# Optimization experiments

Hardware: AMD Instinct MI355X
Metric: run time of the kernel (lower is better)

Reference implementation:

```python
import jax, jax.numpy as jnp
import numpy as np

EMB = 64
HID = 64


def setup_inputs() -> dict:
    key = jax.random.key(0)
    ks = jax.random.split(key, 7)
    obs_len, batch = 20, 65536
    s_in = 1.0 / np.sqrt(2.0)   # torch Linear init scale
    s_h = 1.0 / np.sqrt(HID)    # torch LSTM init scale
    return {
        "obs_traj": jax.random.normal(ks[0], (obs_len, batch, 2), dtype=jnp.float32),
        "W_emb": jax.random.uniform(ks[1], (EMB, 2), jnp.float32, -s_in, s_in),
        "b_emb": jax.random.uniform(ks[2], (EMB,), jnp.float32, -s_in, s_in),
        "W_ih": jax.random.uniform(ks[3], (4 * HID, EMB), jnp.float32, -s_h, s_h),
        "W_hh": jax.random.uniform(ks[4], (4 * HID, HID), jnp.float32, -s_h, s_h),
        "b_ih": jax.random.uniform(ks[5], (4 * HID,), jnp.float32, -s_h, s_h),
        "b_hh": jax.random.uniform(ks[6], (4 * HID,), jnp.float32, -s_h, s_h),
    }


def reference(obs_traj, W_emb, b_emb, W_ih, W_hh, b_ih, b_hh):
    # spatial embedding: (T, B, 2) -> (T, B, EMB)
    emb = jnp.einsum("tbi,ei->tbe", obs_traj, W_emb) + b_emb
    batch = obs_traj.shape[1]
    bias = b_ih + b_hh  # (4H,)
    # precompute input contribution for all timesteps: (T, B, 4H)
    x_gates = jnp.einsum("tbe,ge->tbg", emb, W_ih) + bias

    def step(carry, xg_t):
        h, c = carry
        gates = xg_t + h @ W_hh.T          # (B, 4H)
        i, f, g, o = jnp.split(gates, 4, axis=-1)  # torch gate order i,f,g,o
        i = jax.nn.sigmoid(i)
        f = jax.nn.sigmoid(f)
        g = jnp.tanh(g)
        o = jax.nn.sigmoid(o)
        c_new = f * c + i * g
        h_new = o * jnp.tanh(c_new)
        return (h_new, c_new), None

    h0 = jnp.zeros((batch, HID), dtype=obs_traj.dtype)
    c0 = jnp.zeros((batch, HID), dtype=obs_traj.dtype)
    (h_T, _), _ = jax.lax.scan(step, (h0, c0), x_gates)
    return h_T[None]  # (num_layers=1, batch, h_dim)
```

## Files before the change

kernel.cpp:

```cpp
#include <hip/hip_runtime.h>

#define T_STEPS 20
#define BATCH   65536
#define HIDN    64
#define GATES   256
#define CHUNKS  2
#define HSTR    72

typedef __bf16 bf16x8 __attribute__((ext_vector_type(8)));
typedef float  f32x4  __attribute__((ext_vector_type(4)));
typedef float  f32x2  __attribute__((ext_vector_type(2)));
typedef unsigned int uint32;

#define L2E 1.4426950408889634f

#if __has_builtin(__builtin_amdgcn_exp2f)
#define EXP2F(x) __builtin_amdgcn_exp2f(x)
#else
#define EXP2F(x) exp2f(x)
#endif
#if __has_builtin(__builtin_amdgcn_rcpf)
#define RCPF(x) __builtin_amdgcn_rcpf(x)
#else
#define RCPF(x) (1.0f / (x))
#endif

__device__ __forceinline__ uint32 pack2bf16(float a, float b) {
    unsigned short ua = __builtin_bit_cast(unsigned short, (__bf16)a);
    unsigned short ub = __builtin_bit_cast(unsigned short, (__bf16)b);
    return (uint32)ua | ((uint32)ub << 16);
}

__global__ __launch_bounds__(256, 4)
void Encoder_6949257085628_kernel(const float* __restrict__ obs,
                                  const float* __restrict__ W_emb,
                                  const float* __restrict__ b_emb,
                                  const float* __restrict__ W_ih,
                                  const float* __restrict__ W_hh,
                                  const float* __restrict__ b_ih,
                                  const float* __restrict__ b_hh,
                                  float* __restrict__ out) {
    __shared__ float wcbc[GATES * 3];
    __shared__ __align__(16) __bf16 hlb[2][16 * HSTR];

    const int tid  = threadIdx.x;
    const int jtw  = tid >> 6;
    const int lane = tid & 63;
    const int q    = lane >> 4;
    const int c16  = lane & 15;

    {
        int g = tid;
        float sf = ((g >> 6) == 2) ? (2.0f * L2E) : (-L2E);
        float a0 = 0.f, a1 = 0.f, ab = 0.f;
        for (int e = 0; e < 64; ++e) {
            float wie = W_ih[g * 64 + e];
            a0 = fmaf(wie, W_emb[e * 2 + 0], a0);
            a1 = fmaf(wie, W_emb[e * 2 + 1], a1);
            ab = fmaf(wie, b_emb[e], ab);
        }
        wcbc[g * 3 + 0] = a0 * sf;
        wcbc[g * 3 + 1] = a1 * sf;
        wcbc[g * 3 + 2] = (ab + b_ih[g] + b_hh[g]) * sf;
    }

    bf16x8 bfr[4][2];
    #pragma unroll
    for (int f = 0; f < 4; ++f) {
        const float sf = (f == 2) ? (2.0f * L2E) : (-L2E);
        const int rowW = f * 64 + jtw * 16 + c16;
        #pragma unroll
        for (int ks = 0; ks < 2; ++ks) {
            const float* p = W_hh + rowW * 64 + ks * 32 + q * 8;
            f32x4 lo = *(const f32x4*)p;
            f32x4 hi = *(const f32x4*)(p + 4);
            bf16x8 b;
            b[0] = (__bf16)(lo[0] * sf); b[1] = (__bf16)(lo[1] * sf);
            b[2] = (__bf16)(lo[2] * sf); b[3] = (__bf16)(lo[3] * sf);
            b[4] = (__bf16)(hi[0] * sf); b[5] = (__bf16)(hi[1] * sf);
            b[6] = (__bf16)(hi[2] * sf); b[7] = (__bf16)(hi[3] * sf);
            bfr[f][ks] = b;
        }
    }
    __syncthreads();

    bf16x8 bxf[4];
    f32x4  bcc[4];
    #pragma unroll
    for (int f = 0; f < 4; ++f) {
        int col = f * 64 + jtw * 16 + c16;
        uint32 pk = pack2bf16(wcbc[col * 3 + 0], wcbc[col * 3 + 1]);
        uint32 e0 = (q == 0) ? pk : 0u;
        uint32 z[4] = {e0, 0u, 0u, 0u};
        bxf[f] = __builtin_bit_cast(bf16x8, z);
        float bcs = wcbc[col * 3 + 2];
        bcc[f] = f32x4{bcs, bcs, bcs, bcs};
    }

    const int wgBase = blockIdx.x * (16 * CHUNKS);
    const int hOff   = jtw * 16 + c16;

    #pragma unroll 1
    for (int c = 0; c < CHUNKS; ++c) {
        const int rbw = wgBase + c * 16;
        __syncthreads();

        float cst[4];
        #pragma unroll
        for (int r = 0; r < 4; ++r) cst[r] = 0.f;

        f32x2 xc = *(const f32x2*)&obs[(size_t)(rbw + c16) * 2];
        bf16x8 a0c, a1c;

        auto act_store = [&](f32x4 (&acc)[4], __bf16* hw, bool last) {
            #pragma unroll
            for (int r = 0; r < 4; ++r) {
                float ig = RCPF(1.0f + EXP2F(acc[0][r]));
                float fg = RCPF(1.0f + EXP2F(acc[1][r]));
                float gg = fmaf(-2.0f, RCPF(1.0f + EXP2F(acc[2][r])), 1.0f);
                float og = RCPF(1.0f + EXP2F(acc[3][r]));
                float cc = fmaf(fg, cst[r], ig * gg);
                cst[r] = cc;
                float th = fmaf(-2.0f, RCPF(1.0f + EXP2F(cc * (2.0f * L2E))), 1.0f);
                float h  = og * th;
                if (!last) {
                    hw[(q * 4 + r) * HSTR + hOff] = (__bf16)h;
                } else {
                    out[(size_t)(rbw + q * 4 + r) * HIDN + hOff] = h;
                }
            }
        };
        auto build_ax = [&](f32x2 xv) -> bf16x8 {
            uint32 pk = pack2bf16(xv[0], xv[1]);
            uint32 e0 = (q == 0) ? pk : 0u;
            uint32 z[4] = {e0, 0u, 0u, 0u};
            return __builtin_bit_cast(bf16x8, z);
        };

        {
            bf16x8 ax = build_ax(xc);
            f32x4 acc[4];
            #pragma unroll
            for (int f = 0; f < 4; ++f)
                acc[f] = __builtin_amdgcn_mfma_f32_16x16x32_bf16(ax, bxf[f], bcc[f], 0, 0, 0);
            xc = *(const f32x2*)&obs[(size_t)(BATCH * 2) + (size_t)(rbw + c16) * 2];
            act_store(acc, hlb[0], false);
            __syncthreads();
            a0c = *(const bf16x8*)&hlb[0][c16 * HSTR + q * 8];
            a1c = *(const bf16x8*)&hlb[0][c16 * HSTR + 32 + q * 8];
        }

        #pragma unroll 1
        for (int t = 1; t < T_STEPS - 1; ++t) {
            bf16x8 ax = build_ax(xc);
            f32x4 acc[4];
            #pragma unroll
            for (int f = 0; f < 4; ++f) {
                acc[f] = __builtin_amdgcn_mfma_f32_16x16x32_bf16(ax,  bxf[f],    bcc[f], 0, 0, 0);
                acc[f] = __builtin_amdgcn_mfma_f32_16x16x32_bf16(a0c, bfr[f][0], acc[f], 0, 0, 0);
                acc[f] = __builtin_amdgcn_mfma_f32_16x16x32_bf16(a1c, bfr[f][1], acc[f], 0, 0, 0);
            }
            xc = *(const f32x2*)&obs[(size_t)(t + 1) * (BATCH * 2) + (size_t)(rbw + c16) * 2];
            act_store(acc, hlb[t & 1], false);
            __syncthreads();
            a0c = *(const bf16x8*)&hlb[t & 1][c16 * HSTR + q * 8];
            a1c = *(const bf16x8*)&hlb[t & 1][c16 * HSTR + 32 + q * 8];
        }

        {
            bf16x8 ax = build_ax(xc);
            f32x4 acc[4];
            #pragma unroll
            for (int f = 0; f < 4; ++f) {
                acc[f] = __builtin_amdgcn_mfma_f32_16x16x32_bf16(ax,  bxf[f],    bcc[f], 0, 0, 0);
                acc[f] = __builtin_amdgcn_mfma_f32_16x16x32_bf16(a0c, bfr[f][0], acc[f], 0, 0, 0);
                acc[f] = __builtin_amdgcn_mfma_f32_16x16x32_bf16(a1c, bfr[f][1], acc[f], 0, 0, 0);
            }
            act_store(acc, nullptr, true);
        }
    }
}

extern "C" void kernel_launch(void* const* d_in, const int* in_sizes, int n_in,
                              void* d_out, int out_size, void* d_ws, size_t ws_size,
                              hipStream_t stream) {
    const float* obs   = (const float*)d_in[0];
    const float* W_emb = (const float*)d_in[1];
    const float* b_emb = (const float*)d_in[2];
    const float* W_ih  = (const float*)d_in[3];
    const float* W_hh  = (const float*)d_in[4];
    const float* b_ih  = (const float*)d_in[5];
    const float* b_hh  = (const float*)d_in[6];
    float* out = (float*)d_out;

    dim3 grid(BATCH / (16 * CHUNKS));
    dim3 block(256);
    Encoder_6949257085628_kernel<<<grid, block, 0, stream>>>(
        obs, W_emb, b_emb, W_ih, W_hh, b_ih, b_hh, out);
}
```

Before: 116.9 us.

## Process two 16-row batch tiles per wave and fold bias into MFMA

Each workgroup now handles 32 batch rows per chunk instead of 16, so each wave issues two independent MFMA chains per step. This amortizes the per-step barrier and LDS round trip and gives the scheduler independent work to overlap MFMA with the activation math. The bias is no longer loaded as a replicated accumulator register. It is folded into the input MFMA as a bf16 hi/lo pair multiplied by a constant-one A column, which frees registers. The grid is halved, launch bounds are replaced by waves_per_eu(4,4), and the doubled accumulators and state raise register pressure.

```diff
diff --git a/kernel.cpp b/kernel.cpp
--- a/kernel.cpp
+++ b/kernel.cpp
@@ -11,6 +11,7 @@
 typedef float  f32x4  __attribute__((ext_vector_type(4)));
 typedef float  f32x2  __attribute__((ext_vector_type(2)));
 typedef unsigned int uint32;
+typedef uint32 uint32x4 __attribute__((ext_vector_type(4)));
 
 #define L2E 1.4426950408889634f
 
@@ -31,7 +32,8 @@
     return (uint32)ua | ((uint32)ub << 16);
 }
 
-__global__ __launch_bounds__(256, 4)
+__global__ __launch_bounds__(256)
+__attribute__((amdgpu_waves_per_eu(4, 4)))
 void Encoder_6949257085628_kernel(const float* __restrict__ obs,
                                   const float* __restrict__ W_emb,
                                   const float* __restrict__ b_emb,
@@ -41,13 +43,14 @@
                                   const float* __restrict__ b_hh,
                                   float* __restrict__ out) {
     __shared__ float wcbc[GATES * 3];
-    __shared__ __align__(16) __bf16 hlb[2][16 * HSTR];
+    __shared__ __align__(16) __bf16 hlb[2][32 * HSTR];
 
     const int tid  = threadIdx.x;
     const int jtw  = tid >> 6;
     const int lane = tid & 63;
     const int q    = lane >> 4;
     const int c16  = lane & 15;
+    const bool qz  = (q == 0);
 
     {
         int g = tid;
@@ -84,99 +87,135 @@
     }
     __syncthreads();
 
-    bf16x8 bxf[4];
-    f32x4  bcc[4];
+    uint32 bxw0[4], bxw1[4];
     #pragma unroll
     for (int f = 0; f < 4; ++f) {
         int col = f * 64 + jtw * 16 + c16;
-        uint32 pk = pack2bf16(wcbc[col * 3 + 0], wcbc[col * 3 + 1]);
-        uint32 e0 = (q == 0) ? pk : 0u;
-        uint32 z[4] = {e0, 0u, 0u, 0u};
-        bxf[f] = __builtin_bit_cast(bf16x8, z);
+        float w0s = wcbc[col * 3 + 0];
+        float w1s = wcbc[col * 3 + 1];
         float bcs = wcbc[col * 3 + 2];
-        bcc[f] = f32x4{bcs, bcs, bcs, bcs};
-    }
-
-    const int wgBase = blockIdx.x * (16 * CHUNKS);
+        float blo = bcs - (float)((__bf16)bcs);
+        bxw0[f] = qz ? pack2bf16(w0s, w1s) : 0u;
+        bxw1[f] = qz ? pack2bf16(bcs, blo) : 0u;
+    }
+    const uint32 axw1 = qz ? 0x3F803F80u : 0u;
+
+    const int wgBase = blockIdx.x * (32 * CHUNKS);
     const int hOff   = jtw * 16 + c16;
 
     #pragma unroll 1
     for (int c = 0; c < CHUNKS; ++c) {
-        const int rbw = wgBase + c * 16;
+        const int rbw = wgBase + c * 32;
         __syncthreads();
 
-        float cst[4];
+        float cst[2][4];
         #pragma unroll
-        for (int r = 0; r < 4; ++r) cst[r] = 0.f;
-
-        f32x2 xc = *(const f32x2*)&obs[(size_t)(rbw + c16) * 2];
-        bf16x8 a0c, a1c;
-
-        auto act_store = [&](f32x4 (&acc)[4], __bf16* hw, bool last) {
+        for (int m = 0; m < 2; ++m)
+            #pragma unroll
+            for (int r = 0; r < 4; ++r) cst[m][r] = 0.f;
+
+        f32x2 xc[2];
+        #pragma unroll
+        for (int m = 0; m < 2; ++m)
+            xc[m] = *(const f32x2*)&obs[(size_t)(rbw + m * 16 + c16) * 2];
+
+        auto ax_of = [&](f32x2 xv) -> bf16x8 {
+            uint32 w0 = qz ? pack2bf16(xv[0], xv[1]) : 0u;
+            return __builtin_bit_cast(bf16x8, uint32x4{w0, axw1, 0u, 0u});
+        };
+        auto bx_of = [&](int f) -> bf16x8 {
+            return __builtin_bit_cast(bf16x8, uint32x4{bxw0[f], bxw1[f], 0u, 0u});
+        };
+        auto act_store = [&](f32x4 (&acc)[4], int m, __bf16* hw, bool last) {
             #pragma unroll
             for (int r = 0; r < 4; ++r) {
                 float ig = RCPF(1.0f + EXP2F(acc[0][r]));
                 float fg = RCPF(1.0f + EXP2F(acc[1][r]));
                 float gg = fmaf(-2.0f, RCPF(1.0f + EXP2F(acc[2][r])), 1.0f);
                 float og = RCPF(1.0f + EXP2F(acc[3][r]));
-                float cc = fmaf(fg, cst[r], ig * gg);
-                cst[r] = cc;
+                float cc = fmaf(fg, cst[m][r], ig * gg);
+                cst[m][r] = cc;
                 float th = fmaf(-2.0f, RCPF(1.0f + EXP2F(cc * (2.0f * L2E))), 1.0f);
                 float h  = og * th;
                 if (!last) {
-                    hw[(q * 4 + r) * HSTR + hOff] = (__bf16)h;
+                    hw[(m * 16 + q * 4 + r) * HSTR + hOff] = (__bf16)h;
                 } else {
-                    out[(size_t)(rbw + q * 4 + r) * HIDN + hOff] = h;
+                    out[(size_t)(rbw + m * 16 + q * 4 + r) * HIDN + hOff] = h;
                 }
             }
         };
-        auto build_ax = [&](f32x2 xv) -> bf16x8 {
-            uint32 pk = pack2bf16(xv[0], xv[1]);
-            uint32 e0 = (q == 0) ? pk : 0u;
-            uint32 z[4] = {e0, 0u, 0u, 0u};
-            return __builtin_bit_cast(bf16x8, z);
-        };
+
+        bf16x8 a0c[2], a1c[2];
 
         {
-            bf16x8 ax = build_ax(xc);
-            f32x4 acc[4];
-            #pragma unroll
-            for (int f = 0; f < 4; ++f)
-                acc[f] = __builtin_amdgcn_mfma_f32_16x16x32_bf16(ax, bxf[f], bcc[f], 0, 0, 0);
-            xc = *(const f32x2*)&obs[(size_t)(BATCH * 2) + (size_t)(rbw + c16) * 2];
-            act_store(acc, hlb[0], false);
+            f32x4 acc[2][4];
+            #pragma unroll
+            for (int m = 0; m < 2; ++m) {
+                bf16x8 ax = ax_of(xc[m]);
+                #pragma unroll
+                for (int f = 0; f < 4; ++f)
+                    acc[m][f] = __builtin_amdgcn_mfma_f32_16x16x32_bf16(
+                        ax, bx_of(f), f32x4{0.f, 0.f, 0.f, 0.f}, 0, 0, 0);
+            }
+            #pragma unroll
+            for (int m = 0; m < 2; ++m)
+                xc[m] = *(const f32x2*)&obs[(size_t)(BATCH * 2) + (size_t)(rbw + m * 16 + c16) * 2];
+            act_store(acc[0], 0, hlb[0], false);
+            act_store(acc[1], 1, hlb[0], false);
             __syncthreads();
-            a0c = *(const bf16x8*)&hlb[0][c16 * HSTR + q * 8];
-            a1c = *(const bf16x8*)&hlb[0][c16 * HSTR + 32 + q * 8];
+            #pragma unroll
+            for (int m = 0; m < 2; ++m) {
+                a0c[m] = *(const bf16x8*)&hlb[0][(m * 16 + c16) * HSTR + q * 8];
+                a1c[m] = *(const bf16x8*)&hlb[0][(m * 16 + c16) * HSTR + 32 + q * 8];
+            }
         }
 
         #pragma unroll 1
         for (int t = 1; t < T_STEPS - 1; ++t) {
-            bf16x8 ax = build_ax(xc);
-            f32x4 acc[4];
-            #pragma unroll
-            for (int f = 0; f < 4; ++f) {
-                acc[f] = __builtin_amdgcn_mfma_f32_16x16x32_bf16(ax,  bxf[f],    bcc[f], 0, 0, 0);
-                acc[f] = __builtin_amdgcn_mfma_f32_16x16x32_bf16(a0c, bfr[f][0], acc[f], 0, 0, 0);
-                acc[f] = __builtin_amdgcn_mfma_f32_16x16x32_bf16(a1c, bfr[f][1], acc[f], 0, 0, 0);
-            }
-            xc = *(const f32x2*)&obs[(size_t)(t + 1) * (BATCH * 2) + (size_t)(rbw + c16) * 2];
-            act_store(acc, hlb[t & 1], false);
+            f32x4 acc[2][4];
+            #pragma unroll
+            for (int m = 0; m < 2; ++m) {
+                bf16x8 ax = ax_of(xc[m]);
+                #pragma unroll
+                for (int f = 0; f < 4; ++f) {
+                    acc[m][f] = __builtin_amdgcn_mfma_f32_16x16x32_bf16(
+                        ax, bx_of(f), f32x4{0.f, 0.f, 0.f, 0.f}, 0, 0, 0);
+                    acc[m][f] = __builtin_amdgcn_mfma_f32_16x16x32_bf16(
+                        a0c[m], bfr[f][0], acc[m][f], 0, 0, 0);
+                    acc[m][f] = __builtin_amdgcn_mfma_f32_16x16x32_bf16(
+                        a1c[m], bfr[f][1], acc[m][f], 0, 0, 0);
+                }
+            }
+            #pragma unroll
+            for (int m = 0; m < 2; ++m)
+                xc[m] = *(const f32x2*)&obs[(size_t)(t + 1) * (BATCH * 2) + (size_t)(rbw + m * 16 + c16) * 2];
+            act_store(acc[0], 0, hlb[t & 1], false);
+            act_store(acc[1], 1, hlb[t & 1], false);
             __syncthreads();
-            a0c = *(const bf16x8*)&hlb[t & 1][c16 * HSTR + q * 8];
-            a1c = *(const bf16x8*)&hlb[t & 1][c16 * HSTR + 32 + q * 8];
+            #pragma unroll
+            for (int m = 0; m < 2; ++m) {
+                a0c[m] = *(const bf16x8*)&hlb[t & 1][(m * 16 + c16) * HSTR + q * 8];
+                a1c[m] = *(const bf16x8*)&hlb[t & 1][(m * 16 + c16) * HSTR + 32 + q * 8];
+            }
         }
 
         {
-            bf16x8 ax = build_ax(xc);
-            f32x4 acc[4];
-            #pragma unroll
-            for (int f = 0; f < 4; ++f) {
-                acc[f] = __builtin_amdgcn_mfma_f32_16x16x32_bf16(ax,  bxf[f],    bcc[f], 0, 0, 0);
-                acc[f] = __builtin_amdgcn_mfma_f32_16x16x32_bf16(a0c, bfr[f][0], acc[f], 0, 0, 0);
-                acc[f] = __builtin_amdgcn_mfma_f32_16x16x32_bf16(a1c, bfr[f][1], acc[f], 0, 0, 0);
-            }
-            act_store(acc, nullptr, true);
+            f32x4 acc[2][4];
+            #pragma unroll
+            for (int m = 0; m < 2; ++m) {
+                bf16x8 ax = ax_of(xc[m]);
+                #pragma unroll
+                for (int f = 0; f < 4; ++f) {
+                    acc[m][f] = __builtin_amdgcn_mfma_f32_16x16x32_bf16(
+                        ax, bx_of(f), f32x4{0.f, 0.f, 0.f, 0.f}, 0, 0, 0);
+                    acc[m][f] = __builtin_amdgcn_mfma_f32_16x16x32_bf16(
+                        a0c[m], bfr[f][0], acc[m][f], 0, 0, 0);
+                    acc[m][f] = __builtin_amdgcn_mfma_f32_16x16x32_bf16(
+                        a1c[m], bfr[f][1], acc[m][f], 0, 0, 0);
+                }
+            }
+            act_store(acc[0], 0, nullptr, true);
+            act_store(acc[1], 1, nullptr, true);
         }
     }
 }
@@ -193,7 +232,7 @@
     const float* b_hh  = (const float*)d_in[6];
     float* out = (float*)d_out;
 
-    dim3 grid(BATCH / (16 * CHUNKS));
+    dim3 grid(BATCH / (32 * CHUNKS));
     dim3 block(256);
     Encoder_6949257085628_kernel<<<grid, block, 0, stream>>>(
         obs, W_emb, b_emb, W_ih, W_hh, b_ih, b_hh, out);
```

After: 112.5 us. 1.04x faster.
